# Kernel optimization log

Measured on AMD Instinct MI355X. Metric: run time of the kernel, lower is better.

Reference implementation:

```python
import jax, jax.numpy as jnp
import numpy as np


def setup_inputs() -> dict:
    key = jax.random.key(0)
    k_z, k_w1, k_b1, k_w2, k_b2 = jax.random.split(key, 5)
    latent_dim = 16
    N = 2048
    z = jax.random.normal(k_z, (N, latent_dim), dtype=jnp.float32)
    # torch.nn.Linear default init: U(-1/sqrt(fan_in), 1/sqrt(fan_in))
    lim1 = 1.0 / np.sqrt(2 * latent_dim)
    W1 = jax.random.uniform(k_w1, (2 * latent_dim, latent_dim), minval=-lim1, maxval=lim1, dtype=jnp.float32)
    b1 = jax.random.uniform(k_b1, (latent_dim,), minval=-lim1, maxval=lim1, dtype=jnp.float32)
    lim2 = 1.0 / np.sqrt(latent_dim)
    W2 = jax.random.uniform(k_w2, (latent_dim, 1), minval=-lim2, maxval=lim2, dtype=jnp.float32)
    b2 = jax.random.uniform(k_b2, (1,), minval=-lim2, maxval=lim2, dtype=jnp.float32)
    return {"z": z, "W1": W1, "b1": b1, "W2": W2, "b2": b2}


def reference(z, W1, b1, W2, b2):
    # Pairwise concat is equivalent to splitting W1 into the halves acting on
    # z_i and z_j; we still materialize the [N, N, D] hidden like the original
    # math, but avoid the explicit [N, N, 2D] concat buffer.
    W1_i, W1_j = W1[: z.shape[1]], W1[z.shape[1] :]  # each [D, D_hidden]
    hi = z @ W1_i  # [N, Dh]
    hj = z @ W1_j  # [N, Dh]
    h = jax.nn.relu(hi[:, None, :] + hj[None, :, :] + b1)  # [N, N, Dh]
    logits = h @ W2 + b2  # [N, N, 1]
    return jax.nn.sigmoid(logits[..., 0])  # [N, N]
```

## Files before the change

### kernel.cpp

```cpp
#include <hip/hip_runtime.h>
#include <math.h>

#define D  16
#define JT 256
#define TI 8

typedef _Float16 half2v __attribute__((ext_vector_type(2)));
union H2U { half2v h; unsigned int u; };

__global__ __launch_bounds__(256) void prep_kernel(
    const float* __restrict__ z, const float* __restrict__ W1,
    const float* __restrict__ b1, const float* __restrict__ W2,
    half2v* __restrict__ Hi, half2v* __restrict__ Hj, half2v* __restrict__ w2p)
{
    __shared__ float sZ[16 * D];
    __shared__ float sW[2 * D * D];
    const int tid = threadIdx.x;
    const int rowbase = blockIdx.x * 16;
    if (tid < 64)       ((float4*)sZ)[tid]      = ((const float4*)(z + (size_t)rowbase * D))[tid];
    else if (tid < 192) ((float4*)sW)[tid - 64] = ((const float4*)W1)[tid - 64];
    __syncthreads();

    const int r  = tid >> 4;
    const int u  = tid & 15;
    const int hf = u >> 3;
    const int p  = u & 7;
    const int k0 = 2 * p, k1 = k0 + 1;

    float a0 = 0.f, a1 = 0.f;
    #pragma unroll
    for (int m = 0; m < D; ++m) {
        const float zf = sZ[r * D + m];
        const float* wrow = &sW[(hf * D + m) * D];
        a0 = fmaf(zf, wrow[k0], a0);
        a1 = fmaf(zf, wrow[k1], a1);
    }
    if (hf == 0) { a0 += b1[k0]; a1 += b1[k1]; }

    H2U hv; hv.h.x = (_Float16)a0; hv.h.y = (_Float16)a1;
    (hf ? Hj : Hi)[(size_t)(rowbase + r) * 8 + p] = hv.h;

    if (blockIdx.x == 0 && tid < 8) {
        H2U wv; wv.h.x = (_Float16)W2[2 * tid]; wv.h.y = (_Float16)W2[2 * tid + 1];
        w2p[tid] = wv.h;
    }
}

__global__ __launch_bounds__(256) void MLPDecoder_68092411511098_kernel(
    const half2v* __restrict__ Hi, const half2v* __restrict__ Hj,
    const half2v* __restrict__ w2p, const float* __restrict__ b2,
    float* __restrict__ out, int N)
{
    __shared__ half2v sHi[TI * 8];
    const int tid   = threadIdx.x;
    const int jbase = blockIdx.x * JT;
    const int ibase = blockIdx.y * TI;

    if (tid < TI * 8) sHi[tid] = Hi[(size_t)ibase * 8 + tid];

    half2v vj[8];
    {
        const uint4* src = (const uint4*)(Hj + (size_t)(jbase + tid) * 8);
        union { uint4 q; half2v h[4]; } c0, c1;
        c0.q = src[0]; c1.q = src[1];
        vj[0]=c0.h[0]; vj[1]=c0.h[1]; vj[2]=c0.h[2]; vj[3]=c0.h[3];
        vj[4]=c1.h[0]; vj[5]=c1.h[1]; vj[6]=c1.h[2]; vj[7]=c1.h[3];
    }
    half2v w2v[8];
    #pragma unroll
    for (int p = 0; p < 8; ++p) w2v[p] = w2p[p];
    const float b2s = b2[0];
    const half2v zero = {(_Float16)0.f, (_Float16)0.f};
    __syncthreads();

    float* orow = out + (size_t)ibase * N + jbase + tid;
    #pragma unroll 2
    for (int ii = 0; ii < TI; ++ii) {
        const half2v* hrow = &sHi[ii * 8];
        float acc = b2s;
        #pragma unroll
        for (int p = 0; p < 8; ++p) {
            half2v s = hrow[p] + vj[p];
            half2v r = __builtin_elementwise_max(s, zero);
#if __has_builtin(__builtin_amdgcn_fdot2)
            acc = __builtin_amdgcn_fdot2(r, w2v[p], acc, false);
#else
            acc += (float)r.x * (float)w2v[p].x + (float)r.y * (float)w2v[p].y;
#endif
        }
        const float e = __expf(-acc);
        orow[(size_t)ii * N] = __builtin_amdgcn_rcpf(1.0f + e);
    }
}

extern "C" void kernel_launch(void* const* d_in, const int* in_sizes, int n_in,
                              void* d_out, int out_size, void* d_ws, size_t ws_size,
                              hipStream_t stream) {
    const float* z  = (const float*)d_in[0];
    const float* W1 = (const float*)d_in[1];
    const float* b1 = (const float*)d_in[2];
    const float* W2 = (const float*)d_in[3];
    const float* b2 = (const float*)d_in[4];
    float* out = (float*)d_out;

    const int N = in_sizes[0] / D;

    half2v* Hi  = (half2v*)d_ws;
    half2v* Hj  = Hi + (size_t)N * 8;
    half2v* w2p = Hj + (size_t)N * 8;

    prep_kernel<<<dim3(N / 16), dim3(256), 0, stream>>>(z, W1, b1, W2, Hi, Hj, w2p);

    dim3 grid(N / JT, N / TI);
    MLPDecoder_68092411511098_kernel<<<grid, dim3(256), 0, stream>>>(
        Hi, Hj, w2p, b2, out, N);
}
```

Baseline: 73.46 us.

## Fuse projection prep into main kernel and double rows per block

Removes the separate prep kernel and workspace. Each block now computes its own Hi rows in shared memory and each thread computes its Hj vector from z and W1 in registers. TI grows from 8 to 16 so the recomputation is spread over more output rows, and the unroll goes from 2 to 4. This drops one kernel launch and the workspace round-trip, but every block repeats the Hj projection (256 FMAs per thread) and adds an extra barrier.

Measured after the change: 72.86 us. No clear change (-0.8%).

```diff
diff --git a/kernel.cpp b/kernel.cpp
--- a/kernel.cpp
+++ b/kernel.cpp
@@ -3,78 +3,87 @@
 
 #define D  16
 #define JT 256
-#define TI 8
+#define TI 16
 
 typedef _Float16 half2v __attribute__((ext_vector_type(2)));
 union H2U { half2v h; unsigned int u; };
 
-__global__ __launch_bounds__(256) void prep_kernel(
+__global__ __launch_bounds__(256) void MLPDecoder_68092411511098_kernel(
     const float* __restrict__ z, const float* __restrict__ W1,
     const float* __restrict__ b1, const float* __restrict__ W2,
-    half2v* __restrict__ Hi, half2v* __restrict__ Hj, half2v* __restrict__ w2p)
+    const float* __restrict__ b2, float* __restrict__ out, int N)
 {
-    __shared__ float sZ[16 * D];
-    __shared__ float sW[2 * D * D];
-    const int tid = threadIdx.x;
-    const int rowbase = blockIdx.x * 16;
-    if (tid < 64)       ((float4*)sZ)[tid]      = ((const float4*)(z + (size_t)rowbase * D))[tid];
-    else if (tid < 192) ((float4*)sW)[tid - 64] = ((const float4*)W1)[tid - 64];
-    __syncthreads();
+    __shared__ float  sWi[D * D];
+    __shared__ float  sZi[TI * D];
+    __shared__ float  sB1[D];
+    __shared__ float  sW2[D];
+    __shared__ half2v sHi[TI * 8];
 
-    const int r  = tid >> 4;
-    const int u  = tid & 15;
-    const int hf = u >> 3;
-    const int p  = u & 7;
-    const int k0 = 2 * p, k1 = k0 + 1;
-
-    float a0 = 0.f, a1 = 0.f;
-    #pragma unroll
-    for (int m = 0; m < D; ++m) {
-        const float zf = sZ[r * D + m];
-        const float* wrow = &sW[(hf * D + m) * D];
-        a0 = fmaf(zf, wrow[k0], a0);
-        a1 = fmaf(zf, wrow[k1], a1);
-    }
-    if (hf == 0) { a0 += b1[k0]; a1 += b1[k1]; }
-
-    H2U hv; hv.h.x = (_Float16)a0; hv.h.y = (_Float16)a1;
-    (hf ? Hj : Hi)[(size_t)(rowbase + r) * 8 + p] = hv.h;
-
-    if (blockIdx.x == 0 && tid < 8) {
-        H2U wv; wv.h.x = (_Float16)W2[2 * tid]; wv.h.y = (_Float16)W2[2 * tid + 1];
-        w2p[tid] = wv.h;
-    }
-}
-
-__global__ __launch_bounds__(256) void MLPDecoder_68092411511098_kernel(
-    const half2v* __restrict__ Hi, const half2v* __restrict__ Hj,
-    const half2v* __restrict__ w2p, const float* __restrict__ b2,
-    float* __restrict__ out, int N)
-{
-    __shared__ half2v sHi[TI * 8];
     const int tid   = threadIdx.x;
     const int jbase = blockIdx.x * JT;
     const int ibase = blockIdx.y * TI;
 
-    if (tid < TI * 8) sHi[tid] = Hi[(size_t)ibase * 8 + tid];
+    if (tid < 64)        ((float4*)sWi)[tid]       = ((const float4*)W1)[tid];
+    else if (tid < 128)  ((float4*)sZi)[tid - 64]  = ((const float4*)(z + (size_t)ibase * D))[tid - 64];
+    else if (tid < 132)  ((float4*)sB1)[tid - 128] = ((const float4*)b1)[tid - 128];
+    else if (tid < 136)  ((float4*)sW2)[tid - 132] = ((const float4*)W2)[tid - 132];
+
+    float zr[D];
+    {
+        const float4* zsrc = (const float4*)(z + (size_t)(jbase + tid) * D);
+        const float4 a = zsrc[0], b = zsrc[1], c = zsrc[2], d = zsrc[3];
+        zr[0]=a.x;  zr[1]=a.y;  zr[2]=a.z;  zr[3]=a.w;
+        zr[4]=b.x;  zr[5]=b.y;  zr[6]=b.z;  zr[7]=b.w;
+        zr[8]=c.x;  zr[9]=c.y;  zr[10]=c.z; zr[11]=c.w;
+        zr[12]=d.x; zr[13]=d.y; zr[14]=d.z; zr[15]=d.w;
+    }
+
+    __syncthreads();
+
+    if (tid < TI * 8) {
+        const int r  = tid >> 3;
+        const int p  = tid & 7;
+        const int k0 = 2 * p, k1 = k0 + 1;
+        float a0 = sB1[k0], a1 = sB1[k1];
+        #pragma unroll
+        for (int m = 0; m < D; ++m) {
+            const float zf = sZi[r * D + m];
+            a0 = fmaf(zf, sWi[m * D + k0], a0);
+            a1 = fmaf(zf, sWi[m * D + k1], a1);
+        }
+        H2U hv; hv.h.x = (_Float16)a0; hv.h.y = (_Float16)a1;
+        sHi[r * 8 + p] = hv.h;
+    }
 
     half2v vj[8];
     {
-        const uint4* src = (const uint4*)(Hj + (size_t)(jbase + tid) * 8);
-        union { uint4 q; half2v h[4]; } c0, c1;
-        c0.q = src[0]; c1.q = src[1];
-        vj[0]=c0.h[0]; vj[1]=c0.h[1]; vj[2]=c0.h[2]; vj[3]=c0.h[3];
-        vj[4]=c1.h[0]; vj[5]=c1.h[1]; vj[6]=c1.h[2]; vj[7]=c1.h[3];
+        const float* __restrict__ W1j = W1 + D * D;
+        #pragma unroll
+        for (int p = 0; p < 8; ++p) {
+            float a0 = 0.f, a1 = 0.f;
+            #pragma unroll
+            for (int m = 0; m < D; ++m) {
+                a0 = fmaf(zr[m], W1j[m * D + 2 * p],     a0);
+                a1 = fmaf(zr[m], W1j[m * D + 2 * p + 1], a1);
+            }
+            H2U hv; hv.h.x = (_Float16)a0; hv.h.y = (_Float16)a1;
+            vj[p] = hv.h;
+        }
     }
+
+    __syncthreads();
+
     half2v w2v[8];
     #pragma unroll
-    for (int p = 0; p < 8; ++p) w2v[p] = w2p[p];
+    for (int p = 0; p < 8; ++p) {
+        H2U wv; wv.h.x = (_Float16)sW2[2 * p]; wv.h.y = (_Float16)sW2[2 * p + 1];
+        w2v[p] = wv.h;
+    }
     const float b2s = b2[0];
     const half2v zero = {(_Float16)0.f, (_Float16)0.f};
-    __syncthreads();
 
     float* orow = out + (size_t)ibase * N + jbase + tid;
-    #pragma unroll 2
+    #pragma unroll 4
     for (int ii = 0; ii < TI; ++ii) {
         const half2v* hrow = &sHi[ii * 8];
         float acc = b2s;
@@ -105,13 +114,9 @@
 
     const int N = in_sizes[0] / D;
 
-    half2v* Hi  = (half2v*)d_ws;
-    half2v* Hj  = Hi + (size_t)N * 8;
-    half2v* w2p = Hj + (size_t)N * 8;
-
-    prep_kernel<<<dim3(N / 16), dim3(256), 0, stream>>>(z, W1, b1, W2, Hi, Hj, w2p);
+    (void)d_ws; (void)ws_size;
 
     dim3 grid(N / JT, N / TI);
     MLPDecoder_68092411511098_kernel<<<grid, dim3(256), 0, stream>>>(
-        Hi, Hj, w2p, b2, out, N);
+        z, W1, b1, W2, b2, out, N);
 }
```
